# Performance work log

Hardware: AMD Instinct MI355X
Metric: run time of the kernel (lower is better)

## Reference

```python
import jax, jax.numpy as jnp
import numpy as np

IMAGE_SIZE = 224
BLUR_SIGMA = 4.0  # PIL ImageFilter.GaussianBlur(radius=4): radius acts as std dev
BLUR_RADIUS = 8   # truncate kernel at 2*sigma


def _gaussian_blur(x, sigma=BLUR_SIGMA, radius=BLUR_RADIUS):
    # separable gaussian blur on NCHW, SAME padding
    t = jnp.arange(-radius, radius + 1, dtype=x.dtype)
    kern = jnp.exp(-0.5 * (t / sigma) ** 2)
    kern = kern / kern.sum()
    dn = ('NCHW', 'OIHW', 'NCHW')
    x = jax.lax.conv_general_dilated(x, kern.reshape(1, 1, 1, -1), (1, 1), 'SAME', dimension_numbers=dn)
    x = jax.lax.conv_general_dilated(x, kern.reshape(1, 1, -1, 1), (1, 1), 'SAME', dimension_numbers=dn)
    return x


def setup_inputs() -> dict:
    key = jax.random.key(0)
    ks = jax.random.split(key, 8)
    N = 1000
    inp = {
        'z': jax.random.normal(ks[0], (1, 512), jnp.float32),
        'fmap0': jax.random.normal(ks[1], (1, 64, 56, 56), jnp.float32),
        'fmap1': jax.random.normal(ks[2], (1, 128, 28, 28), jnp.float32),
        'fmap2': jax.random.normal(ks[3], (1, 256, 14, 14), jnp.float32),
        'z_lib': jax.random.normal(ks[4], (N, 512), jnp.float32),
        'lib0': jax.random.normal(ks[5], (N, 64, 56, 56), jnp.float32),
        'lib1': jax.random.normal(ks[6], (N, 128, 28, 28), jnp.float32),
        'lib2': jax.random.normal(ks[7], (N, 256, 14, 14), jnp.float32),
        'k': 5,
    }
    return inp


def reference(z, fmap0, fmap1, fmap2, z_lib, lib0, lib1, lib2, k):
    # distances = ||z_lib - z||_2 over feature dim -> [N]
    dists = jnp.linalg.norm(z_lib - z, axis=1)
    # topk smallest
    neg_vals, indices = jax.lax.top_k(-dists, k)
    z_score = (-neg_vals).mean()

    s_total = jnp.zeros((1, 1, IMAGE_SIZE, IMAGE_SIZE), jnp.float32)
    for fmap, lib in ((fmap0, lib0), (fmap1, lib1), (fmap2, lib2)):
        nearest = lib[indices]                            # [k, C, H, W]
        s = jnp.linalg.norm(nearest - fmap, axis=1)        # [k, H, W] (channel-wise L2)
        s = s.min(axis=0, keepdims=True)                   # [1, H, W]
        s_up = jax.image.resize(s[None], (1, 1, IMAGE_SIZE, IMAGE_SIZE), method='bilinear')
        s_total = s_total + s_up
    s_total = _gaussian_blur(s_total)
    return z_score, s_total
```

## Files before the change

### kernel.cpp

```cpp
#include <hip/hip_runtime.h>
#include <hip/hip_bf16.h>
#include <math.h>

#define IMG 224
#define NLIB 1000
#define ZD 512
#define MAXK 8
#define NTHR 512
#define NBLK 196
#define MTAG 0x5EEDF00Du


__device__ __forceinline__ int clampk(int k) {
    if (k < 1) k = 1;
    if (k > MAXK) k = MAXK;
    return k;
}

__device__ __forceinline__ void cgs_u32(unsigned* p, unsigned v) {
    __hip_atomic_store(p, v, __ATOMIC_RELAXED, __HIP_MEMORY_SCOPE_AGENT);
}
__device__ __forceinline__ unsigned cgl_u32(unsigned* p) {
    return __hip_atomic_load(p, __ATOMIC_RELAXED, __HIP_MEMORY_SCOPE_AGENT);
}
__device__ __forceinline__ void cgs_f32(float* p, float v) {
    __hip_atomic_store(p, v, __ATOMIC_RELAXED, __HIP_MEMORY_SCOPE_AGENT);
}
__device__ __forceinline__ float cgl_f32(const float* p) {
    return __hip_atomic_load((float*)p, __ATOMIC_RELAXED, __HIP_MEMORY_SCOPE_AGENT);
}

__device__ __forceinline__ void barrier_ar(unsigned* slots, int bid, int tid) {
    __syncthreads();
    if (tid == 0) cgs_u32(slots + bid, MTAG);
    if (tid < 64) {
        unsigned pend = 0;
#pragma unroll
        for (int q = 0; q < 4; ++q) { int i = q * 64 + tid; if (i < NBLK) pend |= 1u << q; }
        long guard = 0;
        for (;;) {
#pragma unroll
            for (int q = 0; q < 4; ++q) {
                int i = q * 64 + tid;
                if (pend & (1u << q))
                    if (cgl_u32(slots + i) == MTAG) pend &= ~(1u << q);
            }
            if (__all(pend == 0)) break;
            if (++guard > 100000000L) break;
            __builtin_amdgcn_s_sleep(4);
        }
    }
    __syncthreads();
    asm volatile("" ::: "memory");
}

__device__ __forceinline__ float bilin(const float* __restrict__ msm, int Wl, int Win,
                                       int bx, int by, float scl, int gx, int gy) {
    float sxf = ((float)gx + 0.5f) * scl - 0.5f;
    float syf = ((float)gy + 0.5f) * scl - 0.5f;
    float fx = floorf(sxf), fy = floorf(syf);
    float wx = sxf - fx,    wy = syf - fy;
    int ix = (int)fx, iy = (int)fy;
    int x0c = min(max(ix, 0), Win - 1) - bx, x1c = min(max(ix + 1, 0), Win - 1) - bx;
    int y0c = min(max(iy, 0), Win - 1) - by, y1c = min(max(iy + 1, 0), Win - 1) - by;
    float v00 = msm[y0c * Wl + x0c], v10 = msm[y0c * Wl + x1c];
    float v01 = msm[y1c * Wl + x0c], v11 = msm[y1c * Wl + x1c];
    return (1.f - wy) * ((1.f - wx) * v00 + wx * v10) +
           wy * ((1.f - wx) * v01 + wx * v11);
}

__global__ void __launch_bounds__(NTHR) k_fused(
        const float* __restrict__ z,
        const float* __restrict__ f0, const float* __restrict__ f1,
        const float* __restrict__ f2,
        const float* __restrict__ zlib,
        const float* __restrict__ l0, const float* __restrict__ l1,
        const float* __restrict__ l2,
        const int* __restrict__ kp,
        float* __restrict__ out,
        float* __restrict__ dists, unsigned* __restrict__ a1, unsigned* __restrict__ a2,
        float* __restrict__ s0, float* __restrict__ s1, float* __restrict__ s2) {

    __shared__ float msm0[100], msm1[36], msm2[9];
    __shared__ float pre[32 * 32];
    __shared__ float mid[32 * 16];
    __shared__ float wk[17];

    int tid = threadIdx.x;
    int bid = blockIdx.x;
    int lane = tid & 63, wave = tid >> 6;
    int k = clampk(*kp);

    if (bid == 0 && tid < NBLK) cgs_u32(a2 + tid, 0u);

    if (tid < 17) {
        float r = (float)(tid - 8) * 0.25f;
        wk[tid] = expf(-0.5f * r * r);
    }

    int gw = bid * 8 + wave;
    if (bid < 125 && gw < NLIB) {
        const float4* row4 = (const float4*)(zlib + (size_t)gw * ZD);
        const float4* z4   = (const float4*)z;
        float4 a0 = row4[lane],      b0 = z4[lane];
        float4 a1v = row4[64 + lane], b1v = z4[64 + lane];
        float acc = 0.f, d;
        d = a0.x - b0.x; acc += d * d;  d = a0.y - b0.y; acc += d * d;
        d = a0.z - b0.z; acc += d * d;  d = a0.w - b0.w; acc += d * d;
        d = a1v.x - b1v.x; acc += d * d;  d = a1v.y - b1v.y; acc += d * d;
        d = a1v.z - b1v.z; acc += d * d;  d = a1v.w - b1v.w; acc += d * d;
#pragma unroll
        for (int off = 32; off > 0; off >>= 1) acc += __shfl_xor(acc, off, 64);
        if (lane == 0) cgs_f32(&dists[gw], sqrtf(acc));
    }

    barrier_ar(a1, bid, tid);

    int n0 = k * 1568, n1 = k * 784, n2 = k * 392;
    int njobs = n0 + n1 + n2;
    int j = bid * NTHR + tid;

    const float* fmp = nullptr; const float* lbp = nullptr; float* op = nullptr;
    int kk = 0, pq = 0, cbase = 0, HW = 0, Cfull = 0;
    bool valid = (j < njobs);
    if (valid) {
        if (j < n0) {
            int r = j;           kk = r / 1568; int q = r % 1568;
            int part = q / 784;  pq = q % 784;  cbase = part * 32;
            HW = 3136; Cfull = 64;  fmp = f0; lbp = l0;
            op = s0 + part * (MAXK * 3136) + kk * 3136;
        } else if (j < n0 + n1) {
            int r = j - n0;      kk = r / 784;  int q = r % 784;
            int part = q / 196;  pq = q % 196;  cbase = part * 32;
            HW = 784;  Cfull = 128; fmp = f1; lbp = l1;
            op = s1 + part * (MAXK * 784) + kk * 784;
        } else {
            int r = j - n0 - n1; kk = r / 392;  int q = r % 392;
            int part = q / 49;   pq = q % 49;   cbase = part * 32;
            HW = 196;  Cfull = 256; fmp = f2; lbp = l2;
            op = s2 + part * (MAXK * 196) + kk * 196;
        }
    }

    int waveBase = bid * NTHR + wave * 64;
    bool dotopk = (waveBase < njobs) || (bid == 0 && wave == 0);
    int myidx = 0;
    if (dotopk) {
        float vals[16];
#pragma unroll
        for (int q = 0; q < 16; ++q) {
            int e = lane + 64 * q;
            vals[q] = (e < NLIB) ? cgl_f32(&dists[e]) : 3.4e38f;
        }
        float ssum = 0.f;
        for (int it = 0; it < k; ++it) {
            float bv = 3.4e38f; int bi = 0x7fffffff;
#pragma unroll
            for (int q = 0; q < 16; ++q) {
                if (vals[q] < bv) { bv = vals[q]; bi = lane + 64 * q; }
            }
#pragma unroll
            for (int off = 1; off < 64; off <<= 1) {
                float ov = __shfl_xor(bv, off, 64);
                int   oi = __shfl_xor(bi, off, 64);
                if (ov < bv || (ov == bv && oi < bi)) { bv = ov; bi = oi; }
            }
#pragma unroll
            for (int q = 0; q < 16; ++q) {
                if (lane + 64 * q == bi) vals[q] = 3.4e38f;
            }
            if (it == kk) myidx = bi;
            ssum += bv;
        }
        if (bid == 0 && tid == 0) out[0] = ssum / (float)k;
    }

    if (valid) {
        const float4* lb4 = (const float4*)(lbp + (size_t)myidx * (size_t)Cfull * HW
                                                + (size_t)cbase * HW);
        const float4* fb4 = (const float4*)(fmp + (size_t)cbase * HW);
        int HW4 = HW >> 2;
        float ax = 0.f, ay = 0.f, az = 0.f, aw = 0.f;
#pragma unroll
        for (int c = 0; c < 32; ++c) {
            float4 a = lb4[c * HW4 + pq];
            float4 b = fb4[c * HW4 + pq];
            float dx = a.x - b.x, dy = a.y - b.y, dz = a.z - b.z, dw = a.w - b.w;
            ax += dx * dx; ay += dy * dy; az += dz * dz; aw += dw * dw;
        }
        float* o = op + 4 * pq;
        cgs_f32(o + 0, ax); cgs_f32(o + 1, ay);
        cgs_f32(o + 2, az); cgs_f32(o + 3, aw);
    }

    barrier_ar(a2, bid, tid);

    if (tid == 0) cgs_u32(a1 + bid, 0u);

    int tx = bid % 14, ty = bid / 14;
    int x0 = tx * 16, y0 = ty * 16;
    int b0x = x0 / 4 - 3,  b0y = y0 / 4 - 3;
    int b1x = x0 / 8 - 2,  b1y = y0 / 8 - 2;
    int b2x = x0 / 16 - 1, b2y = y0 / 16 - 1;

    if (tid >= 64 && tid < 64 + 145) {
        int i = tid - 64;
        float m = 3.4e38f;
        if (i < 100) {
            int ly = i / 10, lx = i % 10;
            int gx = min(max(b0x + lx, 0), 55), gy = min(max(b0y + ly, 0), 55);
            int p = gy * 56 + gx;
            for (int kq = 0; kq < k; ++kq) {
                float v = cgl_f32(&s0[kq * 3136 + p])
                        + cgl_f32(&s0[MAXK * 3136 + kq * 3136 + p]);
                m = fminf(m, v);
            }
            msm0[i] = sqrtf(m);
        } else if (i < 136) {
            int r = i - 100; int ly = r / 6, lx = r % 6;
            int gx = min(max(b1x + lx, 0), 27), gy = min(max(b1y + ly, 0), 27);
            int p = gy * 28 + gx;
            for (int kq = 0; kq < k; ++kq) {
                float v = 0.f;
#pragma unroll
                for (int part = 0; part < 4; ++part)
                    v += cgl_f32(&s1[part * (MAXK * 784) + kq * 784 + p]);
                m = fminf(m, v);
            }
            msm1[r] = sqrtf(m);
        } else {
            int r = i - 136; int ly = r / 3, lx = r % 3;
            int gx = min(max(b2x + lx, 0), 13), gy = min(max(b2y + ly, 0), 13);
            int p = gy * 14 + gx;
            for (int kq = 0; kq < k; ++kq) {
                float v = 0.f;
#pragma unroll
                for (int part = 0; part < 8; ++part)
                    v += cgl_f32(&s2[part * (MAXK * 196) + kq * 196 + p]);
                m = fminf(m, v);
            }
            msm2[r] = sqrtf(m);
        }
    }
    __syncthreads();

    float wsum = 0.f;
#pragma unroll
    for (int t = 0; t < 17; ++t) wsum += wk[t];
    float inv2 = 1.f / (wsum * wsum);

    for (int i = tid; i < 32 * 32; i += NTHR) {
        int lx = i % 32, ly = i / 32;
        int gx = x0 - 8 + lx, gy = y0 - 8 + ly;
        float v = 0.f;
        if ((unsigned)gx < (unsigned)IMG && (unsigned)gy < (unsigned)IMG) {
            v = bilin(msm0, 10, 56, b0x, b0y, 0.25f,   gx, gy)
              + bilin(msm1, 6,  28, b1x, b1y, 0.125f,  gx, gy)
              + bilin(msm2, 3,  14, b2x, b2y, 0.0625f, gx, gy);
        }
        pre[i] = v;
    }
    __syncthreads();

    if (tid < 32 * 16) {
        int cx = tid % 16, ly = tid / 16;
        float acc = 0.f;
#pragma unroll
        for (int t = 0; t < 17; ++t) acc += wk[t] * pre[ly * 32 + cx + t];
        mid[ly * 16 + cx] = acc;
    }
    __syncthreads();

    if (tid < 16 * 16) {
        int ox = tid % 16, oy = tid / 16;
        float acc = 0.f;
#pragma unroll
        for (int t = 0; t < 17; ++t) acc += wk[t] * mid[(oy + t) * 16 + ox];
        out[1 + (y0 + oy) * IMG + (x0 + ox)] = acc * inv2;
    }
}

extern "C" void kernel_launch(void* const* d_in, const int* in_sizes, int n_in,
                              void* d_out, int out_size, void* d_ws, size_t ws_size,
                              hipStream_t stream) {
    const float* z    = (const float*)d_in[0];
    const float* f0   = (const float*)d_in[1];
    const float* f1   = (const float*)d_in[2];
    const float* f2   = (const float*)d_in[3];
    const float* zlib = (const float*)d_in[4];
    const float* l0   = (const float*)d_in[5];
    const float* l1   = (const float*)d_in[6];
    const float* l2   = (const float*)d_in[7];
    const int*   kp   = (const int*)d_in[8];
    float* out = (float*)d_out;

    float*    ws    = (float*)d_ws;
    float*    dists = ws;
    unsigned* a1    = (unsigned*)(ws + 1024);
    unsigned* a2    = (unsigned*)(ws + 1280);
    float*    s0    = ws + 1536;
    float*    s1    = s0 + 2 * MAXK * 3136;
    float*    s2    = s1 + 4 * MAXK * 784;

    k_fused<<<NBLK, NTHR, 0, stream>>>(z, f0, f1, f2, zlib, l0, l1, l2, kp,
                                       out, dists, a1, a2, s0, s1, s2);
}
```

Measured before the change: 26.95 us.

## Split fused kernel into distance/top-k kernel and main kernel with centralized barrier

Splits the single persistent kernel into two launches. The first computes the library distances, and one wave waits on per-block flags before doing top-k once and writing the indices to the workspace. The second kernel reads those indices, spreads the gather-distance jobs across blocks wave-by-wave, and replaces the all-to-all grid barrier with a master-release barrier. This removes one grid-wide barrier and the redundant per-wave top-k recomputation, at the cost of an extra kernel launch.

```diff
diff --git a/kernel.cpp b/kernel.cpp
--- a/kernel.cpp
+++ b/kernel.cpp
@@ -7,7 +7,8 @@
 #define ZD 512
 #define MAXK 8
 #define NTHR 512
-#define NBLK 196
+#define KA_BLK 125
+#define KB_BLK 196
 #define MTAG 0x5EEDF00Du
 
 
@@ -30,28 +31,81 @@
     return __hip_atomic_load((float*)p, __ATOMIC_RELAXED, __HIP_MEMORY_SCOPE_AGENT);
 }
 
-__device__ __forceinline__ void barrier_ar(unsigned* slots, int bid, int tid) {
-    __syncthreads();
-    if (tid == 0) cgs_u32(slots + bid, MTAG);
-    if (tid < 64) {
+__global__ void __launch_bounds__(NTHR) k_dist_topk(
+        const float* __restrict__ z, const float* __restrict__ zlib,
+        const int* __restrict__ kp,
+        float* __restrict__ dists, unsigned* __restrict__ d1,
+        int* __restrict__ idxs, float* __restrict__ out) {
+    int tid = threadIdx.x, lane = tid & 63, wave = tid >> 6, bid = blockIdx.x;
+    int k = clampk(*kp);
+
+    int gw = bid * 8 + wave;
+    {
+        const float4* row4 = (const float4*)(zlib + (size_t)gw * ZD);
+        const float4* z4   = (const float4*)z;
+        float4 a0 = row4[lane],      b0 = z4[lane];
+        float4 a1 = row4[64 + lane], b1 = z4[64 + lane];
+        float acc = 0.f, d;
+        d = a0.x - b0.x; acc += d * d;  d = a0.y - b0.y; acc += d * d;
+        d = a0.z - b0.z; acc += d * d;  d = a0.w - b0.w; acc += d * d;
+        d = a1.x - b1.x; acc += d * d;  d = a1.y - b1.y; acc += d * d;
+        d = a1.z - b1.z; acc += d * d;  d = a1.w - b1.w; acc += d * d;
+#pragma unroll
+        for (int off = 32; off > 0; off >>= 1) acc += __shfl_xor(acc, off, 64);
+        if (lane == 0) cgs_f32(&dists[gw], sqrtf(acc));
+    }
+    __syncthreads();
+    if (tid == 0) cgs_u32(d1 + bid, MTAG);
+    if (bid != 0 || wave != 0) return;
+
+    {
         unsigned pend = 0;
 #pragma unroll
-        for (int q = 0; q < 4; ++q) { int i = q * 64 + tid; if (i < NBLK) pend |= 1u << q; }
+        for (int q = 0; q < 2; ++q) { int i = q * 64 + lane; if (i < KA_BLK) pend |= 1u << q; }
         long guard = 0;
         for (;;) {
 #pragma unroll
-            for (int q = 0; q < 4; ++q) {
-                int i = q * 64 + tid;
-                if (pend & (1u << q))
-                    if (cgl_u32(slots + i) == MTAG) pend &= ~(1u << q);
+            for (int q = 0; q < 2; ++q) {
+                int i = q * 64 + lane;
+                if ((pend & (1u << q)) && cgl_u32(d1 + i) == MTAG) pend &= ~(1u << q);
             }
             if (__all(pend == 0)) break;
             if (++guard > 100000000L) break;
-            __builtin_amdgcn_s_sleep(4);
-        }
-    }
-    __syncthreads();
+            __builtin_amdgcn_s_sleep(2);
+        }
+    }
     asm volatile("" ::: "memory");
+
+    float vals[16];
+#pragma unroll
+    for (int q = 0; q < 16; ++q) {
+        int e = lane + 64 * q;
+        vals[q] = (e < NLIB) ? cgl_f32(&dists[e]) : 3.4e38f;
+    }
+    float ssum = 0.f;
+    for (int it = 0; it < k; ++it) {
+        float bv = 3.4e38f; int bi = 0x7fffffff;
+#pragma unroll
+        for (int q = 0; q < 16; ++q) {
+            if (vals[q] < bv) { bv = vals[q]; bi = lane + 64 * q; }
+        }
+#pragma unroll
+        for (int off = 1; off < 64; off <<= 1) {
+            float ov = __shfl_xor(bv, off, 64);
+            int   oi = __shfl_xor(bi, off, 64);
+            if (ov < bv || (ov == bv && oi < bi)) { bv = ov; bi = oi; }
+        }
+#pragma unroll
+        for (int q = 0; q < 16; ++q) {
+            if (lane + 64 * q == bi) vals[q] = 3.4e38f;
+        }
+        if (lane == 0) idxs[it] = bi;
+        ssum += bv;
+    }
+    if (lane == 0) out[0] = ssum / (float)k;
+
+#pragma unroll
+    for (int q = 0; q < 2; ++q) { int i = q * 64 + lane; if (i < KA_BLK) cgs_u32(d1 + i, 0u); }
 }
 
 __device__ __forceinline__ float bilin(const float* __restrict__ msm, int Wl, int Win,
@@ -69,16 +123,14 @@
            wy * ((1.f - wx) * v01 + wx * v11);
 }
 
-__global__ void __launch_bounds__(NTHR) k_fused(
-        const float* __restrict__ z,
+__global__ void __launch_bounds__(NTHR) k_main(
         const float* __restrict__ f0, const float* __restrict__ f1,
         const float* __restrict__ f2,
-        const float* __restrict__ zlib,
         const float* __restrict__ l0, const float* __restrict__ l1,
         const float* __restrict__ l2,
-        const int* __restrict__ kp,
+        const int* __restrict__ idxs, const int* __restrict__ kp,
         float* __restrict__ out,
-        float* __restrict__ dists, unsigned* __restrict__ a1, unsigned* __restrict__ a2,
+        unsigned* __restrict__ b1, unsigned* __restrict__ rel,
         float* __restrict__ s0, float* __restrict__ s1, float* __restrict__ s2) {
 
     __shared__ float msm0[100], msm1[36], msm2[9];
@@ -86,116 +138,88 @@
     __shared__ float mid[32 * 16];
     __shared__ float wk[17];
 
-    int tid = threadIdx.x;
-    int bid = blockIdx.x;
-    int lane = tid & 63, wave = tid >> 6;
+    int tid = threadIdx.x, lane = tid & 63, wv = tid >> 6, bid = blockIdx.x;
     int k = clampk(*kp);
-
-    if (bid == 0 && tid < NBLK) cgs_u32(a2 + tid, 0u);
 
     if (tid < 17) {
         float r = (float)(tid - 8) * 0.25f;
         wk[tid] = expf(-0.5f * r * r);
     }
 
-    int gw = bid * 8 + wave;
-    if (bid < 125 && gw < NLIB) {
-        const float4* row4 = (const float4*)(zlib + (size_t)gw * ZD);
-        const float4* z4   = (const float4*)z;
-        float4 a0 = row4[lane],      b0 = z4[lane];
-        float4 a1v = row4[64 + lane], b1v = z4[64 + lane];
-        float acc = 0.f, d;
-        d = a0.x - b0.x; acc += d * d;  d = a0.y - b0.y; acc += d * d;
-        d = a0.z - b0.z; acc += d * d;  d = a0.w - b0.w; acc += d * d;
-        d = a1v.x - b1v.x; acc += d * d;  d = a1v.y - b1v.y; acc += d * d;
-        d = a1v.z - b1v.z; acc += d * d;  d = a1v.w - b1v.w; acc += d * d;
-#pragma unroll
-        for (int off = 32; off > 0; off >>= 1) acc += __shfl_xor(acc, off, 64);
-        if (lane == 0) cgs_f32(&dists[gw], sqrtf(acc));
-    }
-
-    barrier_ar(a1, bid, tid);
-
     int n0 = k * 1568, n1 = k * 784, n2 = k * 392;
     int njobs = n0 + n1 + n2;
-    int j = bid * NTHR + tid;
-
-    const float* fmp = nullptr; const float* lbp = nullptr; float* op = nullptr;
-    int kk = 0, pq = 0, cbase = 0, HW = 0, Cfull = 0;
-    bool valid = (j < njobs);
-    if (valid) {
-        if (j < n0) {
-            int r = j;           kk = r / 1568; int q = r % 1568;
-            int part = q / 784;  pq = q % 784;  cbase = part * 32;
-            HW = 3136; Cfull = 64;  fmp = f0; lbp = l0;
-            op = s0 + part * (MAXK * 3136) + kk * 3136;
-        } else if (j < n0 + n1) {
-            int r = j - n0;      kk = r / 784;  int q = r % 784;
-            int part = q / 196;  pq = q % 196;  cbase = part * 32;
-            HW = 784;  Cfull = 128; fmp = f1; lbp = l1;
-            op = s1 + part * (MAXK * 784) + kk * 784;
-        } else {
-            int r = j - n0 - n1; kk = r / 392;  int q = r % 392;
-            int part = q / 49;   pq = q % 49;   cbase = part * 32;
-            HW = 196;  Cfull = 256; fmp = f2; lbp = l2;
-            op = s2 + part * (MAXK * 196) + kk * 196;
-        }
-    }
-
-    int waveBase = bid * NTHR + wave * 64;
-    bool dotopk = (waveBase < njobs) || (bid == 0 && wave == 0);
-    int myidx = 0;
-    if (dotopk) {
-        float vals[16];
-#pragma unroll
-        for (int q = 0; q < 16; ++q) {
-            int e = lane + 64 * q;
-            vals[q] = (e < NLIB) ? cgl_f32(&dists[e]) : 3.4e38f;
-        }
-        float ssum = 0.f;
-        for (int it = 0; it < k; ++it) {
-            float bv = 3.4e38f; int bi = 0x7fffffff;
-#pragma unroll
-            for (int q = 0; q < 16; ++q) {
-                if (vals[q] < bv) { bv = vals[q]; bi = lane + 64 * q; }
-            }
-#pragma unroll
-            for (int off = 1; off < 64; off <<= 1) {
-                float ov = __shfl_xor(bv, off, 64);
-                int   oi = __shfl_xor(bi, off, 64);
-                if (ov < bv || (ov == bv && oi < bi)) { bv = ov; bi = oi; }
-            }
-#pragma unroll
-            for (int q = 0; q < 16; ++q) {
-                if (lane + 64 * q == bi) vals[q] = 3.4e38f;
-            }
-            if (it == kk) myidx = bi;
-            ssum += bv;
-        }
-        if (bid == 0 && tid == 0) out[0] = ssum / (float)k;
-    }
-
-    if (valid) {
-        const float4* lb4 = (const float4*)(lbp + (size_t)myidx * (size_t)Cfull * HW
-                                                + (size_t)cbase * HW);
-        const float4* fb4 = (const float4*)(fmp + (size_t)cbase * HW);
-        int HW4 = HW >> 2;
-        float ax = 0.f, ay = 0.f, az = 0.f, aw = 0.f;
-#pragma unroll
-        for (int c = 0; c < 32; ++c) {
-            float4 a = lb4[c * HW4 + pq];
-            float4 b = fb4[c * HW4 + pq];
-            float dx = a.x - b.x, dy = a.y - b.y, dz = a.z - b.z, dw = a.w - b.w;
-            ax += dx * dx; ay += dy * dy; az += dz * dz; aw += dw * dw;
-        }
-        float* o = op + 4 * pq;
-        cgs_f32(o + 0, ax); cgs_f32(o + 1, ay);
-        cgs_f32(o + 2, az); cgs_f32(o + 3, aw);
-    }
-
-    barrier_ar(a2, bid, tid);
-
-    if (tid == 0) cgs_u32(a1 + bid, 0u);
+    int nwj = (njobs + 63) >> 6;
+    int s = bid + KB_BLK * wv;
+    if (s < nwj) {
+        int j = s * 64 + lane;
+        if (j < njobs) {
+            const float* fmp; const float* lbp; float* op;
+            int kk, pq, cbase, HW, Cfull;
+            if (j < n0) {
+                int r = j;           kk = r / 1568; int q = r % 1568;
+                int part = q / 784;  pq = q % 784;  cbase = part * 32;
+                HW = 3136; Cfull = 64;  fmp = f0; lbp = l0;
+                op = s0 + part * (MAXK * 3136) + kk * 3136;
+            } else if (j < n0 + n1) {
+                int r = j - n0;      kk = r / 784;  int q = r % 784;
+                int part = q / 196;  pq = q % 196;  cbase = part * 32;
+                HW = 784;  Cfull = 128; fmp = f1; lbp = l1;
+                op = s1 + part * (MAXK * 784) + kk * 784;
+            } else {
+                int r = j - n0 - n1; kk = r / 392;  int q = r % 392;
+                int part = q / 49;   pq = q % 49;   cbase = part * 32;
+                HW = 196;  Cfull = 256; fmp = f2; lbp = l2;
+                op = s2 + part * (MAXK * 196) + kk * 196;
+            }
+            int myidx = idxs[kk];
+            const float4* lb4 = (const float4*)(lbp + (size_t)myidx * (size_t)Cfull * HW
+                                                    + (size_t)cbase * HW);
+            const float4* fb4 = (const float4*)(fmp + (size_t)cbase * HW);
+            int HW4 = HW >> 2;
+            float ax = 0.f, ay = 0.f, az = 0.f, aw = 0.f;
+#pragma unroll
+            for (int c = 0; c < 32; ++c) {
+                float4 a = lb4[c * HW4 + pq];
+                float4 b = fb4[c * HW4 + pq];
+                float dx = a.x - b.x, dy = a.y - b.y, dz = a.z - b.z, dw = a.w - b.w;
+                ax += dx * dx; ay += dy * dy; az += dz * dz; aw += dw * dw;
+            }
+            float* o = op + 4 * pq;
+            cgs_f32(o + 0, ax); cgs_f32(o + 1, ay);
+            cgs_f32(o + 2, az); cgs_f32(o + 3, aw);
+        }
+    }
+
+    __syncthreads();
+    if (tid == 0) cgs_u32(b1 + bid, MTAG);
+    if (bid == 0 && tid < 64) {
+        unsigned pend = 0;
+#pragma unroll
+        for (int q = 0; q < 4; ++q) { int i = q * 64 + tid; if (i < KB_BLK) pend |= 1u << q; }
+        long guard = 0;
+        for (;;) {
+#pragma unroll
+            for (int q = 0; q < 4; ++q) {
+                int i = q * 64 + tid;
+                if ((pend & (1u << q)) && cgl_u32(b1 + i) == MTAG) pend &= ~(1u << q);
+            }
+            if (__all(pend == 0)) break;
+            if (++guard > 100000000L) break;
+            __builtin_amdgcn_s_sleep(2);
+        }
+#pragma unroll
+        for (int q = 0; q < 4; ++q) { int i = q * 64 + tid; if (i < KB_BLK) cgs_u32(rel + i, MTAG); }
+    }
+    if (tid == 0) {
+        long guard = 0;
+        while (cgl_u32(rel + bid) != MTAG) {
+            if (++guard > 100000000L) break;
+            __builtin_amdgcn_s_sleep(2);
+        }
+    }
+    __syncthreads();
+    asm volatile("" ::: "memory");
+    if (tid == 0) { cgs_u32(rel + bid, 0u); cgs_u32(b1 + bid, 0u); }
 
     int tx = bid % 14, ty = bid / 14;
     int x0 = tx * 16, y0 = ty * 16;
@@ -296,12 +320,15 @@
 
     float*    ws    = (float*)d_ws;
     float*    dists = ws;
-    unsigned* a1    = (unsigned*)(ws + 1024);
-    unsigned* a2    = (unsigned*)(ws + 1280);
-    float*    s0    = ws + 1536;
+    unsigned* d1    = (unsigned*)(ws + 1000);
+    int*      idxs  = (int*)(ws + 1152);
+    unsigned* b1    = (unsigned*)(ws + 1184);
+    unsigned* rel   = (unsigned*)(ws + 1408);
+    float*    s0    = ws + 1664;
     float*    s1    = s0 + 2 * MAXK * 3136;
     float*    s2    = s1 + 4 * MAXK * 784;
 
-    k_fused<<<NBLK, NTHR, 0, stream>>>(z, f0, f1, f2, zlib, l0, l1, l2, kp,
-                                       out, dists, a1, a2, s0, s1, s2);
-}
+    k_dist_topk<<<KA_BLK, NTHR, 0, stream>>>(z, zlib, kp, dists, d1, idxs, out);
+    k_main<<<KB_BLK, NTHR, 0, stream>>>(f0, f1, f2, l0, l1, l2, idxs, kp, out,
+                                        b1, rel, s0, s1, s2);
+}
```

Result: faster. 23.87 us (-11.4%).
